# Kernel optimization log

Measured on AMD Instinct MI355X. Metric: run time of the kernel, lower is better.

The kernel has to match this reference:

```python
import jax, jax.numpy as jnp
import numpy as np

B, T, NQ, NK = 2, 8, 128, 128
DIM_IN, DIM_OUT = 64, 256


def setup_inputs() -> dict:
    key = jax.random.key(0)
    ks = jax.random.split(key, 6)
    scale = 0.05  # keep tanh out of full saturation
    return {
        "query": jax.random.normal(ks[0], (B, NQ, DIM_IN), dtype=jnp.float32),
        "keys": jax.random.normal(ks[1], (B, T, NK, DIM_IN), dtype=jnp.float32),
        "Wq": jax.random.normal(ks[2], (DIM_IN, DIM_OUT), dtype=jnp.float32) * scale,
        "Wk": jax.random.normal(ks[3], (DIM_IN, DIM_OUT), dtype=jnp.float32) * scale,
        "bk": jax.random.normal(ks[4], (DIM_OUT,), dtype=jnp.float32) * scale,
        "v": jax.random.normal(ks[5], (DIM_OUT,), dtype=jnp.float32) * scale,
    }


def reference(query, keys, Wq, Wk, bk, v):
    # q: [B, Nq, D], k: [B, T, Nk, D]
    q = jnp.einsum("bqi,id->bqd", query, Wq)
    k = jnp.einsum("btki,id->btkd", keys, Wk) + bk
    # broadcast add -> [B, T, Nq, Nk, D], tanh, then score projection D->1
    h = jnp.tanh(q[:, None, :, None, :] + k[:, :, None, :, :])
    scores = jnp.einsum("btqkd,d->btqk", h, v)
    return jax.nn.softmax(scores, axis=-1)
```

## Files before the change

### kernel.cpp

```cpp
#include <hip/hip_runtime.h>

#define C_TANH 2.8853900817779268f

__global__ __launch_bounds__(256) void kproj_kernel(
    const float* __restrict__ keys, const float* __restrict__ Wk,
    const float* __restrict__ bk, float* __restrict__ k2) {
  int bid = blockIdx.x;
  int bt  = bid >> 4;
  int kg  = bid & 15;
  int d   = threadIdx.x;
  __shared__ float4 krows4[128];

  if (threadIdx.x < 128)
    krows4[threadIdx.x] =
        ((const float4*)(keys + bt * 8192 + kg * 512))[threadIdx.x];
  __syncthreads();

  float acc[8];
  float bias = bk[d];
#pragma unroll
  for (int kk = 0; kk < 8; ++kk) acc[kk] = bias;

#pragma unroll 4
  for (int i4 = 0; i4 < 16; ++i4) {
    float wa = Wk[(i4 * 4 + 0) * 256 + d];
    float wb = Wk[(i4 * 4 + 1) * 256 + d];
    float wc = Wk[(i4 * 4 + 2) * 256 + d];
    float wd = Wk[(i4 * 4 + 3) * 256 + d];
#pragma unroll
    for (int kk = 0; kk < 8; ++kk) {
      float4 kr = krows4[kk * 16 + i4];
      acc[kk] = fmaf(kr.x, wa, acc[kk]);
      acc[kk] = fmaf(kr.y, wb, acc[kk]);
      acc[kk] = fmaf(kr.z, wc, acc[kk]);
      acc[kk] = fmaf(kr.w, wd, acc[kk]);
    }
  }
#pragma unroll
  for (int kk = 0; kk < 8; ++kk)
    k2[(bt * 256 + d) * 128 + kg * 8 + kk] = acc[kk] * C_TANH;
}

__global__ __launch_bounds__(256) void score_kernel(
    const float* __restrict__ query, const float* __restrict__ Wq,
    const float* __restrict__ v, const float* __restrict__ k2,
    float* __restrict__ out) {
  __shared__ float2 qv[2][256];
  __shared__ float qrow[2][64];
  __shared__ float redm[4], reds[4];
  int tid = threadIdx.x;
  int r   = tid >> 7;
  int k   = tid & 127;
  int wid = tid >> 6;
  int g0  = blockIdx.x * 2;
  int bt  = g0 >> 7;
  int b   = g0 >> 10;
  int q0  = b * 128 + (g0 & 127);

  if (tid < 128) qrow[tid >> 6][tid & 63] = query[q0 * 64 + tid];
  __syncthreads();

  for (int idx = tid; idx < 512; idx += 256) {
    int rr = idx >> 8;
    int d  = idx & 255;
    float acc = 0.f;
#pragma unroll
    for (int i = 0; i < 64; ++i) acc += qrow[rr][i] * Wq[i * 256 + d];
    qv[rr][d] = make_float2(acc * C_TANH, v[d]);
  }
  __syncthreads();

  const float* kp = k2 + bt * 256 * 128 + k;
  float acc = 0.f;
#pragma unroll 8
  for (int d = 0; d < 256; ++d) {
    float2 t = qv[r][d];
    float x  = t.x + kp[d * 128];
    float e  = __builtin_amdgcn_exp2f(x);
    acc += t.y * __builtin_amdgcn_rcpf(1.0f + e);
  }
  float s = -C_TANH * acc;

  float m = s;
#pragma unroll
  for (int off = 32; off > 0; off >>= 1) m = fmaxf(m, __shfl_xor(m, off, 64));
  if ((tid & 63) == 0) redm[wid] = m;
  __syncthreads();
  float rowm = fmaxf(redm[r * 2], redm[r * 2 + 1]);

  float e = __builtin_amdgcn_exp2f(s - rowm);
  float ssum = e;
#pragma unroll
  for (int off = 32; off > 0; off >>= 1) ssum += __shfl_xor(ssum, off, 64);
  if ((tid & 63) == 0) reds[wid] = ssum;
  __syncthreads();
  float tot = reds[r * 2] + reds[r * 2 + 1];

  out[(g0 + r) * 128 + k] = e * __builtin_amdgcn_rcpf(tot);
}

extern "C" void kernel_launch(void* const* d_in, const int* in_sizes, int n_in,
                              void* d_out, int out_size, void* d_ws, size_t ws_size,
                              hipStream_t stream) {
  const float* query = (const float*)d_in[0];
  const float* keys  = (const float*)d_in[1];
  const float* Wq    = (const float*)d_in[2];
  const float* Wk    = (const float*)d_in[3];
  const float* bk    = (const float*)d_in[4];
  const float* v     = (const float*)d_in[5];
  float* out = (float*)d_out;

  float* k2 = (float*)d_ws;

  kproj_kernel<<<256, 256, 0, stream>>>(keys, Wk, bk, k2);
  score_kernel<<<1024, 256, 0, stream>>>(query, Wq, v, k2, out);
}
```

Measured before the change: 91.60 us.

## Precompute query projection once and process two keys per thread in score kernel

Moves the query projection out of the score kernel into the projection kernel, so each query row is projected once instead of being recomputed in every (b,t) block. The score kernel now handles four query rows per block, with each thread computing two keys through float2 loads. The softmax reduction stays within a single wavefront, so the shared-memory reductions and barriers go away. In exchange, the projected query is written to and read back from workspace, and the block count halves, which lowers the number of waves in flight.

Result: faster. 89.13 us (-2.7%).

```diff
diff --git a/kernel.cpp b/kernel.cpp
--- a/kernel.cpp
+++ b/kernel.cpp
@@ -2,101 +2,104 @@
 
 #define C_TANH 2.8853900817779268f
 
-__global__ __launch_bounds__(256) void kproj_kernel(
-    const float* __restrict__ keys, const float* __restrict__ Wk,
-    const float* __restrict__ bk, float* __restrict__ k2) {
+__global__ __launch_bounds__(256) void proj_kernel(
+    const float* __restrict__ query, const float* __restrict__ keys,
+    const float* __restrict__ Wq, const float* __restrict__ Wk,
+    const float* __restrict__ bk, float* __restrict__ q1,
+    float* __restrict__ k2) {
   int bid = blockIdx.x;
-  int bt  = bid >> 4;
-  int kg  = bid & 15;
   int d   = threadIdx.x;
-  __shared__ float4 krows4[128];
+  if (bid < 256) {
+    int bt = bid >> 4;
+    int kg = bid & 15;
+    __shared__ float4 krows4[128];
+    if (threadIdx.x < 128)
+      krows4[threadIdx.x] =
+          ((const float4*)(keys + bt * 8192 + kg * 512))[threadIdx.x];
+    __syncthreads();
 
-  if (threadIdx.x < 128)
-    krows4[threadIdx.x] =
-        ((const float4*)(keys + bt * 8192 + kg * 512))[threadIdx.x];
-  __syncthreads();
-
-  float acc[8];
-  float bias = bk[d];
+    float acc[8];
+    float bias = bk[d];
 #pragma unroll
-  for (int kk = 0; kk < 8; ++kk) acc[kk] = bias;
-
+    for (int kk = 0; kk < 8; ++kk) acc[kk] = bias;
 #pragma unroll 4
-  for (int i4 = 0; i4 < 16; ++i4) {
-    float wa = Wk[(i4 * 4 + 0) * 256 + d];
-    float wb = Wk[(i4 * 4 + 1) * 256 + d];
-    float wc = Wk[(i4 * 4 + 2) * 256 + d];
-    float wd = Wk[(i4 * 4 + 3) * 256 + d];
+    for (int i4 = 0; i4 < 16; ++i4) {
+      float wa = Wk[(i4 * 4 + 0) * 256 + d];
+      float wb = Wk[(i4 * 4 + 1) * 256 + d];
+      float wc = Wk[(i4 * 4 + 2) * 256 + d];
+      float wd = Wk[(i4 * 4 + 3) * 256 + d];
 #pragma unroll
-    for (int kk = 0; kk < 8; ++kk) {
-      float4 kr = krows4[kk * 16 + i4];
-      acc[kk] = fmaf(kr.x, wa, acc[kk]);
-      acc[kk] = fmaf(kr.y, wb, acc[kk]);
-      acc[kk] = fmaf(kr.z, wc, acc[kk]);
-      acc[kk] = fmaf(kr.w, wd, acc[kk]);
+      for (int kk = 0; kk < 8; ++kk) {
+        float4 kr = krows4[kk * 16 + i4];
+        acc[kk] = fmaf(kr.x, wa, acc[kk]);
+        acc[kk] = fmaf(kr.y, wb, acc[kk]);
+        acc[kk] = fmaf(kr.z, wc, acc[kk]);
+        acc[kk] = fmaf(kr.w, wd, acc[kk]);
+      }
     }
+#pragma unroll
+    for (int kk = 0; kk < 8; ++kk)
+      k2[(bt * 256 + d) * 128 + kg * 8 + kk] = acc[kk] * C_TANH;
+  } else {
+    int row = bid - 256;
+    __shared__ float qrow[64];
+    if (threadIdx.x < 64) qrow[threadIdx.x] = query[row * 64 + threadIdx.x];
+    __syncthreads();
+    float acc = 0.f;
+#pragma unroll
+    for (int i = 0; i < 64; ++i) acc += qrow[i] * Wq[i * 256 + d];
+    q1[row * 256 + d] = acc * C_TANH;
   }
-#pragma unroll
-  for (int kk = 0; kk < 8; ++kk)
-    k2[(bt * 256 + d) * 128 + kg * 8 + kk] = acc[kk] * C_TANH;
 }
 
 __global__ __launch_bounds__(256) void score_kernel(
-    const float* __restrict__ query, const float* __restrict__ Wq,
-    const float* __restrict__ v, const float* __restrict__ k2,
-    float* __restrict__ out) {
-  __shared__ float2 qv[2][256];
-  __shared__ float qrow[2][64];
-  __shared__ float redm[4], reds[4];
+    const float* __restrict__ q1, const float* __restrict__ v,
+    const float* __restrict__ k2, float* __restrict__ out) {
+  __shared__ float2 qv[4][256];
   int tid = threadIdx.x;
-  int r   = tid >> 7;
-  int k   = tid & 127;
-  int wid = tid >> 6;
-  int g0  = blockIdx.x * 2;
+  int r   = tid >> 6;
+  int kk  = tid & 63;
+  int g0  = blockIdx.x * 4;
   int bt  = g0 >> 7;
   int b   = g0 >> 10;
-  int q0  = b * 128 + (g0 & 127);
+  int q1base = b * 128 + (g0 & 127);
 
-  if (tid < 128) qrow[tid >> 6][tid & 63] = query[q0 * 64 + tid];
-  __syncthreads();
-
-  for (int idx = tid; idx < 512; idx += 256) {
+  for (int idx = tid; idx < 1024; idx += 256) {
     int rr = idx >> 8;
     int d  = idx & 255;
-    float acc = 0.f;
-#pragma unroll
-    for (int i = 0; i < 64; ++i) acc += qrow[rr][i] * Wq[i * 256 + d];
-    qv[rr][d] = make_float2(acc * C_TANH, v[d]);
+    qv[rr][d] = make_float2(q1[(q1base + rr) * 256 + d], v[d]);
   }
   __syncthreads();
 
-  const float* kp = k2 + bt * 256 * 128 + k;
-  float acc = 0.f;
+  const float2* kp2 = (const float2*)(k2 + bt * 32768) + kk;
+  float acc0 = 0.f, acc1 = 0.f;
 #pragma unroll 8
   for (int d = 0; d < 256; ++d) {
-    float2 t = qv[r][d];
-    float x  = t.x + kp[d * 128];
-    float e  = __builtin_amdgcn_exp2f(x);
-    acc += t.y * __builtin_amdgcn_rcpf(1.0f + e);
+    float2 qvv = qv[r][d];
+    float2 kv  = kp2[d * 64];
+    float x0 = qvv.x + kv.x;
+    float x1 = qvv.x + kv.y;
+    float e0 = __builtin_amdgcn_exp2f(x0);
+    float e1 = __builtin_amdgcn_exp2f(x1);
+    float r0 = __builtin_amdgcn_rcpf(1.0f + e0);
+    float r1 = __builtin_amdgcn_rcpf(1.0f + e1);
+    acc0 = fmaf(qvv.y, r0, acc0);
+    acc1 = fmaf(qvv.y, r1, acc1);
   }
-  float s = -C_TANH * acc;
+  float s0 = -C_TANH * acc0;
+  float s1 = -C_TANH * acc1;
 
-  float m = s;
+  float m = fmaxf(s0, s1);
 #pragma unroll
   for (int off = 32; off > 0; off >>= 1) m = fmaxf(m, __shfl_xor(m, off, 64));
-  if ((tid & 63) == 0) redm[wid] = m;
-  __syncthreads();
-  float rowm = fmaxf(redm[r * 2], redm[r * 2 + 1]);
-
-  float e = __builtin_amdgcn_exp2f(s - rowm);
-  float ssum = e;
+  float e0 = __builtin_amdgcn_exp2f(s0 - m);
+  float e1 = __builtin_amdgcn_exp2f(s1 - m);
+  float ssum = e0 + e1;
 #pragma unroll
   for (int off = 32; off > 0; off >>= 1) ssum += __shfl_xor(ssum, off, 64);
-  if ((tid & 63) == 0) reds[wid] = ssum;
-  __syncthreads();
-  float tot = reds[r * 2] + reds[r * 2 + 1];
+  float inv = __builtin_amdgcn_rcpf(ssum);
 
-  out[(g0 + r) * 128 + k] = e * __builtin_amdgcn_rcpf(tot);
+  ((float2*)(out + (g0 + r) * 128))[kk] = make_float2(e0 * inv, e1 * inv);
 }
 
 extern "C" void kernel_launch(void* const* d_in, const int* in_sizes, int n_in,
@@ -110,8 +113,10 @@
   const float* v     = (const float*)d_in[5];
   float* out = (float*)d_out;
 
-  float* k2 = (float*)d_ws;
+  float* ws = (float*)d_ws;
+  float* q1 = ws;
+  float* k2 = ws + 65536;
 
-  kproj_kernel<<<256, 256, 0, stream>>>(keys, Wk, bk, k2);
-  score_kernel<<<1024, 256, 0, stream>>>(query, Wq, v, k2, out);
+  proj_kernel<<<512, 256, 0, stream>>>(query, keys, Wq, Wk, bk, q1, k2);
+  score_kernel<<<512, 256, 0, stream>>>(q1, v, k2, out);
 }
```
